# Kernel tuning notes

Hardware: AMD Instinct MI355X
Metric: run time of the kernel (lower is better)

Reference implementation:

```python
import jax, jax.numpy as jnp
import numpy as np

B, NP, K, E = 8, 4096, 1024, 262144   # graphs, nodes/graph, topk keep, edges
N = B * NP
EPS = 1e-5


def _glorot(k, fi, fo):
    lim = float(np.sqrt(6.0 / (fi + fo)))
    return jax.random.uniform(k, (fi, fo), jnp.float32, -lim, lim)


def setup_inputs() -> dict:
    key = jax.random.key(0)
    ks = jax.random.split(key, 16)
    pos = jax.random.normal(ks[0], (N, 3), jnp.float32)
    epg = E // B
    src = jax.random.randint(ks[1], (E,), 0, NP)
    dst = jax.random.randint(ks[2], (E,), 0, NP)
    off = jnp.repeat(jnp.arange(B) * NP, epg)   # edges stay within their graph
    edge_index = jnp.stack([src + off, dst + off]).astype(jnp.int32)
    batch = jnp.repeat(jnp.arange(B, dtype=jnp.int32), NP)
    inp = {"pos": pos, "edge_index": edge_index, "batch": batch,
           "p": jax.random.normal(ks[3], (3,), jnp.float32)}
    dims = [3, 64, 128, 128, 256, 512]
    for i in range(5):
        fi, fo = dims[i], dims[i + 1]
        inp[f"W{i+1}"] = _glorot(ks[4 + i], fi, fo)
        inp[f"b{i+1}"] = jnp.zeros((fo,), jnp.float32)
        inp[f"g{i+1}"] = jnp.ones((fo,), jnp.float32)
        inp[f"be{i+1}"] = jnp.zeros((fo,), jnp.float32)
    for i, (fi, fo) in enumerate([(512, 256), (256, 256), (256, 100)]):
        inp[f"fw{i+1}"] = _glorot(ks[9 + i], fi, fo)
        inp[f"fb{i+1}"] = jnp.zeros((fo,), jnp.float32)
    return inp


def _bn(x, g, b):
    # BatchNorm1d in training mode: batch stats over the node dim
    m = jnp.mean(x, 0)
    v = jnp.var(x, 0)
    return (x - m) * jax.lax.rsqrt(v + EPS) * g + b


def _gcn(x, src, dst, ew, W, bb, n):
    # GCNConv with add_self_loops=True, symmetric normalization.
    h = x @ W                                              # [n, out]
    deg = jax.ops.segment_sum(ew, dst, num_segments=n) + 1.0  # +1 self-loop
    dinv = jax.lax.rsqrt(deg)
    norm = dinv[src] * ew * dinv[dst]                      # masked edges -> 0
    agg = jax.ops.segment_sum(h[src] * norm[:, None], dst, num_segments=n)
    return agg + h * (dinv * dinv)[:, None] + bb           # self-loop term + bias


def _forward(pos, p, W1, b1, g1, be1, W2, b2, g2, be2, W3, b3, g3, be3,
             W4, b4, g4, be4, W5, b5, g5, be5, fw1, fb1, fw2, fb2, fw3, fb3,
             edge_index):
    # --- TopKPooling(ratio=1024): projection score, tanh, top-k per graph ---
    s = jnp.tanh(pos @ p / jnp.linalg.norm(p))             # [N]
    vals, idx = jax.lax.top_k(s.reshape(B, NP), K)         # [B,K]
    perm = (idx + (jnp.arange(B) * NP)[:, None]).reshape(-1)
    x = pos[perm] * vals.reshape(-1)[:, None]              # gate kept nodes
    Nn = B * K
    remap = jnp.full((N,), -1, jnp.int32).at[perm].set(jnp.arange(Nn, dtype=jnp.int32))
    src, dst = remap[edge_index[0]], remap[edge_index[1]]
    valid = (src >= 0) & (dst >= 0)
    ew = valid.astype(x.dtype)                             # 0-weight == removed edge
    src = jnp.where(valid, src, 0)
    dst = jnp.where(valid, dst, 0)
    for (W, bb, g, be) in ((W1, b1, g1, be1), (W2, b2, g2, be2),
                           (W3, b3, g3, be3), (W4, b4, g4, be4),
                           (W5, b5, g5, be5)):
        x = jax.nn.relu(_bn(_gcn(x, src, dst, ew, W, bb, Nn), g, be))
    # --- global sum pooling (torch_scatter default reduce='sum') ---
    batch_new = jnp.repeat(jnp.arange(B), K)
    x = jax.ops.segment_sum(x, batch_new, num_segments=B)  # [B,512]
    x = jax.nn.relu(x @ fw1 + fb1)
    x = jax.nn.relu(x @ fw2 + fb2)
    return jax.nn.log_softmax(x @ fw3 + fb3, axis=-1)      # [B,100]


def reference(pos, edge_index, batch, p, W1, b1, g1, be1, W2, b2, g2, be2,
              W3, b3, g3, be3, W4, b4, g4, be4, W5, b5, g5, be5,
              fw1, fb1, fw2, fb2, fw3, fb3):
    del batch  # graph ids are the fixed contiguous layout encoded in B, NP, K
    return _forward(pos, p, W1, b1, g1, be1, W2, b2, g2, be2, W3, b3, g3, be3,
                    W4, b4, g4, be4, W5, b5, g5, be5,
                    fw1, fb1, fw2, fb2, fw3, fb3, edge_index)
```

## Files before the change

kernel.cpp:

```cpp
#include <hip/hip_runtime.h>
#include <math.h>

#define NTOT 32768
#define NPG  4096
#define BGR  8
#define KK   1024
#define NN   8192
#define NE   262144

typedef __attribute__((ext_vector_type(8))) short bf16x8;
typedef __attribute__((ext_vector_type(4))) float f32x4;

static __device__ __forceinline__ unsigned short f2bf(float f) {
    unsigned u = __float_as_uint(f);
    return (unsigned short)((u + 0x7fffu + ((u >> 16) & 1u)) >> 16);
}
static __device__ __forceinline__ float bf2f(unsigned short b) {
    return __uint_as_float(((unsigned)b) << 16);
}

__global__ __launch_bounds__(1024) void k_topk2(const float* __restrict__ pos,
                                                const float* __restrict__ p,
                                                int* __restrict__ remap,
                                                float* __restrict__ x0f,
                                                unsigned short* __restrict__ Ab0,
                                                int* __restrict__ deg,
                                                int* __restrict__ cursor) {
    __shared__ unsigned skey[NPG];
    __shared__ float sval[NPG];
    __shared__ int hist[256];
    __shared__ int Sarr[256];
    __shared__ int wsum[16];
    __shared__ int s_bin, s_above;

    const int g = blockIdx.x, tid = threadIdx.x;
    const int lane = tid & 63, wid = tid >> 6;
    deg[g * KK + tid] = 0;
    cursor[g * KK + tid] = 0;
    const float p0 = p[0], p1 = p[1], p2 = p[2];
    const float invn = 1.0f / sqrtf(p0 * p0 + p1 * p1 + p2 * p2);

    for (int i = tid; i < NPG; i += 1024) {
        const float* pp = pos + (size_t)(g * NPG + i) * 3;
        float s = tanhf((pp[0] * p0 + pp[1] * p1 + pp[2] * p2) * invn);
        sval[i] = s;
        unsigned b = __float_as_uint(s);
        skey[i] = (b & 0x80000000u) ? ~b : (b | 0x80000000u);
    }
    __syncthreads();

    unsigned prefix = 0;
    int needed = KK;
    for (int r = 0; r < 4; ++r) {
        const int sh = 24 - 8 * r;
        if (tid < 256) hist[tid] = 0;
        __syncthreads();
        for (int i = tid; i < NPG; i += 1024) {
            unsigned k = skey[i];
            bool act = (r == 0) || ((k >> (sh + 8)) == prefix);
            if (act) atomicAdd(&hist[(k >> sh) & 255u], 1);
        }
        __syncthreads();
        if (wid == 0) {
            int h0 = hist[4 * lane + 0], h1 = hist[4 * lane + 1];
            int h2 = hist[4 * lane + 2], h3 = hist[4 * lane + 3];
            int l3 = h3, l2 = h2 + l3, l1 = h1 + l2, l0 = h0 + l1;
            int t = l0;
            for (int off = 1; off < 64; off <<= 1) {
                int n = __shfl_down(t, off, 64);
                if (lane + off < 64) t += n;
            }
            int hi = t - l0;
            Sarr[4 * lane + 0] = l0 + hi;
            Sarr[4 * lane + 1] = l1 + hi;
            Sarr[4 * lane + 2] = l2 + hi;
            Sarr[4 * lane + 3] = l3 + hi;
        }
        __syncthreads();
        if (tid < 256) {
            int Sb = Sarr[tid];
            int Sb1 = (tid < 255) ? Sarr[tid + 1] : 0;
            if (Sb >= needed && Sb1 < needed) { s_bin = tid; s_above = Sb1; }
        }
        __syncthreads();
        needed -= s_above;
        prefix = (prefix << 8) | (unsigned)s_bin;
        __syncthreads();
    }
    const unsigned Tkey = prefix;
    const int needTies = needed;

    int tiebase = 0, keepbase = 0;
    for (int c = 0; c < 4; ++c) {
        const int i = c * 1024 + tid;
        const unsigned k = skey[i];
        const int tie = (k == Tkey) ? 1 : 0;
        int v = tie;
        for (int off = 1; off < 64; off <<= 1) {
            int n = __shfl_up(v, off, 64);
            if (lane >= off) v += n;
        }
        if (lane == 63) wsum[wid] = v;
        __syncthreads();
        if (wid == 0) {
            int w = (lane < 16) ? wsum[lane] : 0;
            for (int off = 1; off < 16; off <<= 1) {
                int n = __shfl_up(w, off, 64);
                if (lane >= off) w += n;
            }
            if (lane < 16) wsum[lane] = w;
        }
        __syncthreads();
        const int trank = tiebase + v + (wid > 0 ? wsum[wid - 1] : 0) - tie;
        const int ttot = wsum[15];
        const int keep = (k > Tkey) || (tie && trank < needTies);
        __syncthreads();
        int u = keep;
        for (int off = 1; off < 64; off <<= 1) {
            int n = __shfl_up(u, off, 64);
            if (lane >= off) u += n;
        }
        if (lane == 63) wsum[wid] = u;
        __syncthreads();
        if (wid == 0) {
            int w = (lane < 16) ? wsum[lane] : 0;
            for (int off = 1; off < 16; off <<= 1) {
                int n = __shfl_up(w, off, 64);
                if (lane >= off) w += n;
            }
            if (lane < 16) wsum[lane] = w;
        }
        __syncthreads();
        const int kincl = u + (wid > 0 ? wsum[wid - 1] : 0);
        const int ktot = wsum[15];
        if (keep) {
            int nn = g * KK + keepbase + kincl - 1;
            remap[g * NPG + i] = nn;
            float val = sval[i];
            const float* pp = pos + (size_t)(g * NPG + i) * 3;
            float v0 = pp[0] * val, v1 = pp[1] * val, v2 = pp[2] * val;
            x0f[(size_t)nn * 3 + 0] = v0;
            x0f[(size_t)nn * 3 + 1] = v1;
            x0f[(size_t)nn * 3 + 2] = v2;
            unsigned short* rw = Ab0 + (size_t)nn * 32;
            ushort4 a = make_ushort4(f2bf(v0), f2bf(v1), f2bf(v2), 0);
            ushort4 z = make_ushort4(0, 0, 0, 0);
            *(ushort4*)(rw) = a;
#pragma unroll
            for (int t = 1; t < 8; ++t) *(ushort4*)(rw + 4 * t) = z;
        } else {
            remap[g * NPG + i] = -1;
        }
        tiebase += ttot;
        keepbase += ktot;
        __syncthreads();
    }
}

__global__ void k_deg(const int* __restrict__ ei, const int* __restrict__ remap,
                      int* __restrict__ deg) {
    int e = blockIdx.x * blockDim.x + threadIdx.x;
    if (e >= NE) return;
    int s = remap[ei[e]];
    int d = remap[ei[NE + e]];
    if (s >= 0 && d >= 0) atomicAdd(&deg[d], 1);
}

__global__ __launch_bounds__(1024) void k_scan(const int* __restrict__ deg,
                                               int* __restrict__ rowptr) {
    __shared__ int part[1024];
    const int tid = threadIdx.x;
    const int base = tid * 8;
    int loc[8];
    int s = 0;
#pragma unroll
    for (int i = 0; i < 8; ++i) { loc[i] = s; s += deg[base + i]; }
    part[tid] = s;
    __syncthreads();
    for (int off = 1; off < 1024; off <<= 1) {
        int v = (tid >= off) ? part[tid - off] : 0;
        __syncthreads();
        part[tid] += v;
        __syncthreads();
    }
    int pre = (tid > 0) ? part[tid - 1] : 0;
#pragma unroll
    for (int i = 0; i < 8; ++i) rowptr[base + i] = pre + loc[i];
    if (tid == 1023) rowptr[NN] = pre + s;
}

__global__ void k_place2(const int* __restrict__ ei, const int* __restrict__ remap,
                         const int* __restrict__ deg, const int* __restrict__ rowptr,
                         int* __restrict__ cursor, int* __restrict__ col,
                         float* __restrict__ ew) {
    int e = blockIdx.x * blockDim.x + threadIdx.x;
    if (e >= NE) return;
    int s = remap[ei[e]];
    int d = remap[ei[NE + e]];
    if (s >= 0 && d >= 0) {
        int pos = rowptr[d] + atomicAdd(&cursor[d], 1);
        col[pos] = s;
        ew[pos] = rsqrtf((float)(deg[s] + 1)) * rsqrtf((float)(deg[d] + 1));
    }
}

__global__ void k_wt_all(const float* __restrict__ w0, const float* __restrict__ w1,
                         const float* __restrict__ w2, const float* __restrict__ w3,
                         const float* __restrict__ w4,
                         unsigned short* __restrict__ t0, unsigned short* __restrict__ t1,
                         unsigned short* __restrict__ t2, unsigned short* __restrict__ t3,
                         unsigned short* __restrict__ t4) {
    int i = blockIdx.x * blockDim.x + threadIdx.x;
    const float* W; unsigned short* T; int Kd, Nc, Kpad, base;
    if (i < 2048)        { W = w0; T = t0; Kd = 3;   Nc = 64;  Kpad = 32;  base = 0; }
    else if (i < 10240)  { W = w1; T = t1; Kd = 64;  Nc = 128; Kpad = 64;  base = 2048; }
    else if (i < 26624)  { W = w2; T = t2; Kd = 128; Nc = 128; Kpad = 128; base = 10240; }
    else if (i < 59392)  { W = w3; T = t3; Kd = 128; Nc = 256; Kpad = 128; base = 26624; }
    else if (i < 190464) { W = w4; T = t4; Kd = 256; Nc = 512; Kpad = 256; base = 59392; }
    else return;
    int j = i - base;
    int n = j / Kpad, k = j - n * Kpad;
    float v = (k < Kd) ? W[(size_t)k * Nc + n] : 0.0f;
    T[j] = f2bf(v);
}

__global__ __launch_bounds__(256) void k_mm2(const unsigned short* __restrict__ Ab,
                                             const float* __restrict__ Yin,
                                             const float* __restrict__ scale,
                                             const float* __restrict__ shift,
                                             const unsigned short* __restrict__ WT,
                                             unsigned short* __restrict__ Hb,
                                             int Kd, int Nc) {
    const int lane = threadIdx.x & 63, wid = threadIdx.x >> 6;
    const int bm = blockIdx.x * 64 + (wid >> 1) * 32;
    const int bn = blockIdx.y * 64 + (wid & 1) * 32;
    const int fr = lane & 15;
    const int ko = (lane >> 4) << 3;
    const int row0 = bm + fr;
    const unsigned short* B0 = WT + (size_t)(bn + fr) * Kd + ko;
    const size_t strA = (size_t)16 * Kd;
    f32x4 acc00 = {0,0,0,0}, acc01 = {0,0,0,0}, acc10 = {0,0,0,0}, acc11 = {0,0,0,0};
    for (int k0 = 0; k0 < Kd; k0 += 32) {
        bf16x8 a0, a1;
        if (Yin) {
            const int cc = ko + k0;
            const float4 sc0 = *(const float4*)&scale[cc];
            const float4 sc1 = *(const float4*)&scale[cc + 4];
            const float4 sh0 = *(const float4*)&shift[cc];
            const float4 sh1 = *(const float4*)&shift[cc + 4];
            const float* y0 = Yin + (size_t)row0 * Kd + cc;
            const float* y1 = y0 + strA;
#pragma unroll
            for (int h = 0; h < 2; ++h) {
                const float* yy = h ? y1 : y0;
                float4 u = *(const float4*)yy;
                float4 v = *(const float4*)(yy + 4);
                bf16x8 a;
                a[0] = (short)f2bf(fmaxf(u.x * sc0.x + sh0.x, 0.0f));
                a[1] = (short)f2bf(fmaxf(u.y * sc0.y + sh0.y, 0.0f));
                a[2] = (short)f2bf(fmaxf(u.z * sc0.z + sh0.z, 0.0f));
                a[3] = (short)f2bf(fmaxf(u.w * sc0.w + sh0.w, 0.0f));
                a[4] = (short)f2bf(fmaxf(v.x * sc1.x + sh1.x, 0.0f));
                a[5] = (short)f2bf(fmaxf(v.y * sc1.y + sh1.y, 0.0f));
                a[6] = (short)f2bf(fmaxf(v.z * sc1.z + sh1.z, 0.0f));
                a[7] = (short)f2bf(fmaxf(v.w * sc1.w + sh1.w, 0.0f));
                if (h) a1 = a; else a0 = a;
            }
        } else {
            const unsigned short* A0 = Ab + (size_t)row0 * Kd + ko + k0;
            a0 = *(const bf16x8*)A0;
            a1 = *(const bf16x8*)(A0 + strA);
        }
        bf16x8 b0 = *(const bf16x8*)(B0 + k0);
        bf16x8 b1 = *(const bf16x8*)(B0 + strA + k0);
        acc00 = __builtin_amdgcn_mfma_f32_16x16x32_bf16(b0, a0, acc00, 0, 0, 0);
        acc01 = __builtin_amdgcn_mfma_f32_16x16x32_bf16(b1, a0, acc01, 0, 0, 0);
        acc10 = __builtin_amdgcn_mfma_f32_16x16x32_bf16(b0, a1, acc10, 0, 0, 0);
        acc11 = __builtin_amdgcn_mfma_f32_16x16x32_bf16(b1, a1, acc11, 0, 0, 0);
    }
    const int r = lane & 15;
    const int c4 = (lane >> 4) << 2;
#pragma unroll
    for (int tm = 0; tm < 2; ++tm) {
        const int row = bm + tm * 16 + r;
        const size_t basep = (size_t)row * Nc;
        const f32x4 aL = tm ? acc10 : acc00;
        const f32x4 aR = tm ? acc11 : acc01;
#pragma unroll
        for (int tn = 0; tn < 2; ++tn) {
            const f32x4 a = tn ? aR : aL;
            const int c = bn + tn * 16 + c4;
            *(ushort4*)&Hb[basep + c] = make_ushort4(f2bf(a[0]), f2bf(a[1]),
                                                     f2bf(a[2]), f2bf(a[3]));
        }
    }
}

__global__ __launch_bounds__(256) void k_mm2w(const float* __restrict__ Yin,
                                              const float* __restrict__ scale,
                                              const float* __restrict__ shift,
                                              const unsigned short* __restrict__ WT,
                                              unsigned short* __restrict__ Hb,
                                              int Kd, int Nc) {
    const int lane = threadIdx.x & 63, wid = threadIdx.x >> 6;
    const int bm = blockIdx.x * 64 + (wid >> 1) * 32;
    const int bn = blockIdx.y * 128 + (wid & 1) * 32;
    const int fr = lane & 15;
    const int ko = (lane >> 4) << 3;
    const int row0 = bm + fr;
    const unsigned short* B0 = WT + (size_t)(bn + fr) * Kd + ko;
    const unsigned short* B2 = WT + (size_t)(bn + 64 + fr) * Kd + ko;
    const size_t strA = (size_t)16 * Kd;
    f32x4 acc00 = {0,0,0,0}, acc01 = {0,0,0,0}, acc10 = {0,0,0,0}, acc11 = {0,0,0,0};
    f32x4 acc20 = {0,0,0,0}, acc21 = {0,0,0,0}, acc30 = {0,0,0,0}, acc31 = {0,0,0,0};
    for (int k0 = 0; k0 < Kd; k0 += 32) {
        bf16x8 a0, a1;
        {
            const int cc = ko + k0;
            const float4 sc0 = *(const float4*)&scale[cc];
            const float4 sc1 = *(const float4*)&scale[cc + 4];
            const float4 sh0 = *(const float4*)&shift[cc];
            const float4 sh1 = *(const float4*)&shift[cc + 4];
            const float* y0 = Yin + (size_t)row0 * Kd + cc;
            const float* y1 = y0 + strA;
#pragma unroll
            for (int h = 0; h < 2; ++h) {
                const float* yy = h ? y1 : y0;
                float4 u = *(const float4*)yy;
                float4 v = *(const float4*)(yy + 4);
                bf16x8 a;
                a[0] = (short)f2bf(fmaxf(u.x * sc0.x + sh0.x, 0.0f));
                a[1] = (short)f2bf(fmaxf(u.y * sc0.y + sh0.y, 0.0f));
                a[2] = (short)f2bf(fmaxf(u.z * sc0.z + sh0.z, 0.0f));
                a[3] = (short)f2bf(fmaxf(u.w * sc0.w + sh0.w, 0.0f));
                a[4] = (short)f2bf(fmaxf(v.x * sc1.x + sh1.x, 0.0f));
                a[5] = (short)f2bf(fmaxf(v.y * sc1.y + sh1.y, 0.0f));
                a[6] = (short)f2bf(fmaxf(v.z * sc1.z + sh1.z, 0.0f));
                a[7] = (short)f2bf(fmaxf(v.w * sc1.w + sh1.w, 0.0f));
                if (h) a1 = a; else a0 = a;
            }
        }
        bf16x8 b0 = *(const bf16x8*)(B0 + k0);
        bf16x8 b1 = *(const bf16x8*)(B0 + strA + k0);
        bf16x8 b2 = *(const bf16x8*)(B2 + k0);
        bf16x8 b3 = *(const bf16x8*)(B2 + strA + k0);
        acc00 = __builtin_amdgcn_mfma_f32_16x16x32_bf16(b0, a0, acc00, 0, 0, 0);
        acc01 = __builtin_amdgcn_mfma_f32_16x16x32_bf16(b1, a0, acc01, 0, 0, 0);
        acc10 = __builtin_amdgcn_mfma_f32_16x16x32_bf16(b0, a1, acc10, 0, 0, 0);
        acc11 = __builtin_amdgcn_mfma_f32_16x16x32_bf16(b1, a1, acc11, 0, 0, 0);
        acc20 = __builtin_amdgcn_mfma_f32_16x16x32_bf16(b2, a0, acc20, 0, 0, 0);
        acc21 = __builtin_amdgcn_mfma_f32_16x16x32_bf16(b3, a0, acc21, 0, 0, 0);
        acc30 = __builtin_amdgcn_mfma_f32_16x16x32_bf16(b2, a1, acc30, 0, 0, 0);
        acc31 = __builtin_amdgcn_mfma_f32_16x16x32_bf16(b3, a1, acc31, 0, 0, 0);
    }
    const int r = lane & 15;
    const int c4 = (lane >> 4) << 2;
#pragma unroll
    for (int ct = 0; ct < 2; ++ct) {
#pragma unroll
        for (int tm = 0; tm < 2; ++tm) {
            const int row = bm + tm * 16 + r;
            const size_t basep = (size_t)row * Nc;
            f32x4 aL, aR;
            if (ct == 0) { aL = tm ? acc10 : acc00; aR = tm ? acc11 : acc01; }
            else         { aL = tm ? acc30 : acc20; aR = tm ? acc31 : acc21; }
#pragma unroll
            for (int tn = 0; tn < 2; ++tn) {
                const f32x4 a = tn ? aR : aL;
                const int c = bn + ct * 64 + tn * 16 + c4;
                *(ushort4*)&Hb[basep + c] = make_ushort4(f2bf(a[0]), f2bf(a[1]),
                                                         f2bf(a[2]), f2bf(a[3]));
            }
        }
    }
}

#define BM 64
#define BNT 64
#define BKT 16
__global__ __launch_bounds__(256) void k_mm(const float* __restrict__ A,
                                            const float* __restrict__ W,
                                            float* __restrict__ H, int Kd, int Nc) {
    __shared__ float As[BM][BKT + 1];
    __shared__ float Bs[BKT][BNT + 1];
    const int bm = blockIdx.x * BM;
    const int bn = blockIdx.y * BNT;
    const int tid = threadIdx.x;
    const int tx = tid & 15, ty = tid >> 4;
    float acc[4][4] = {};
    for (int k0 = 0; k0 < Kd; k0 += BKT) {
        for (int t = 0; t < 4; ++t) {
            int i = tid + t * 256;
            int m = i >> 4, k = i & 15;
            As[m][k] = (k0 + k < Kd) ? A[(size_t)(bm + m) * Kd + k0 + k] : 0.0f;
        }
        for (int t = 0; t < 4; ++t) {
            int i = tid + t * 256;
            int k = i >> 6, n = i & 63;
            Bs[k][n] = (k0 + k < Kd) ? W[(size_t)(k0 + k) * Nc + bn + n] : 0.0f;
        }
        __syncthreads();
        for (int k = 0; k < BKT; ++k) {
            float a[4], b[4];
#pragma unroll
            for (int i = 0; i < 4; ++i) a[i] = As[ty * 4 + i][k];
#pragma unroll
            for (int j = 0; j < 4; ++j) b[j] = Bs[k][tx * 4 + j];
#pragma unroll
            for (int i = 0; i < 4; ++i)
#pragma unroll
                for (int j = 0; j < 4; ++j) acc[i][j] += a[i] * b[j];
        }
        __syncthreads();
    }
#pragma unroll
    for (int i = 0; i < 4; ++i)
        *(float4*)&H[(size_t)(bm + ty * 4 + i) * Nc + bn + tx * 4] =
            make_float4(acc[i][0], acc[i][1], acc[i][2], acc[i][3]);
}

#define BN1_ROWS 16
#define BN1_CHUNKS (NN / BN1_ROWS)
__global__ __launch_bounds__(256) void k_gfuse(const unsigned short* __restrict__ Hb,
                                               const float* __restrict__ Hf,
                                               const int* __restrict__ rowptr,
                                               const int* __restrict__ col,
                                               const float* __restrict__ ew,
                                               const int* __restrict__ deg,
                                               const float* __restrict__ bias,
                                               float* __restrict__ Y,
                                               float* __restrict__ psum,
                                               float* __restrict__ psq, int Nc) {
    __shared__ float4 ls[256], lq[256];
    const int CHB = (Nc < 128) ? Nc : 128;
    const int CB = Nc / CHB;
    const int chunk = blockIdx.x / CB;
    const int cb = blockIdx.x - chunk * CB;
    const int QPB = CHB >> 2;
    const int tid = threadIdx.x;
    const int q = tid & (QPB - 1);
    const int rg = tid / QPB;
    const int NRG = 256 / QPB;
    const int RPT = BN1_ROWS / NRG;
    const int c = cb * CHB + (q << 2);
    const float4 b4 = *(const float4*)&bias[c];
    float4 s4 = make_float4(0, 0, 0, 0), q4 = make_float4(0, 0, 0, 0);
    for (int rr = 0; rr < RPT; ++rr) {
        const int n = chunk * BN1_ROWS + rg * RPT + rr;
        const int j0 = rowptr[n], j1 = rowptr[n + 1];
        const float inv = 1.0f / (float)(deg[n] + 1);
        float4 acc;
        if (Hb) {
            ushort4 hv = *(const ushort4*)&Hb[(size_t)n * Nc + c];
            acc = make_float4(bf2f(hv.x), bf2f(hv.y), bf2f(hv.z), bf2f(hv.w));
        } else {
            acc = *(const float4*)&Hf[(size_t)n * Nc + c];
        }
        acc.x = acc.x * inv + b4.x;
        acc.y = acc.y * inv + b4.y;
        acc.z = acc.z * inv + b4.z;
        acc.w = acc.w * inv + b4.w;
        if (Hb) {
            for (int j = j0; j < j1; ++j) {
                const float w = ew[j];
                ushort4 hv = *(const ushort4*)&Hb[(size_t)col[j] * Nc + c];
                acc.x += bf2f(hv.x) * w; acc.y += bf2f(hv.y) * w;
                acc.z += bf2f(hv.z) * w; acc.w += bf2f(hv.w) * w;
            }
        } else {
            for (int j = j0; j < j1; ++j) {
                const float w = ew[j];
                const float4 hv = *(const float4*)&Hf[(size_t)col[j] * Nc + c];
                acc.x += hv.x * w; acc.y += hv.y * w; acc.z += hv.z * w; acc.w += hv.w * w;
            }
        }
        *(float4*)&Y[(size_t)n * Nc + c] = acc;
        s4.x += acc.x; s4.y += acc.y; s4.z += acc.z; s4.w += acc.w;
        q4.x += acc.x * acc.x; q4.y += acc.y * acc.y;
        q4.z += acc.z * acc.z; q4.w += acc.w * acc.w;
    }
    ls[tid] = s4; lq[tid] = q4;
    __syncthreads();
    for (int st = 128; st >= QPB; st >>= 1) {
        if (tid < st) {
            float4 a = ls[tid], b = ls[tid + st];
            ls[tid] = make_float4(a.x + b.x, a.y + b.y, a.z + b.z, a.w + b.w);
            float4 e = lq[tid], f = lq[tid + st];
            lq[tid] = make_float4(e.x + f.x, e.y + f.y, e.z + f.z, e.w + f.w);
        }
        __syncthreads();
    }
    if (tid < QPB) {
        *(float4*)&psum[(size_t)chunk * Nc + c] = ls[tid];
        *(float4*)&psq[(size_t)chunk * Nc + c] = lq[tid];
    }
}

__global__ __launch_bounds__(256) void k_bn2p(const float* __restrict__ psum,
                                              const float* __restrict__ psq,
                                              const float* __restrict__ g,
                                              const float* __restrict__ be,
                                              float* __restrict__ scale,
                                              float* __restrict__ shift, int Nc) {
    __shared__ float ss[256], sq[256];
    const int c = blockIdx.x;
    const int t = threadIdx.x;
    float s = 0.0f, q = 0.0f;
    for (int b = t; b < BN1_CHUNKS; b += 256) {
        s += psum[(size_t)b * Nc + c];
        q += psq[(size_t)b * Nc + c];
    }
    ss[t] = s; sq[t] = q;
    __syncthreads();
    for (int st = 128; st > 0; st >>= 1) {
        if (t < st) { ss[t] += ss[t + st]; sq[t] += sq[t + st]; }
        __syncthreads();
    }
    if (t == 0) {
        double mean = (double)ss[0] / 8192.0;
        double var = (double)sq[0] / 8192.0 - mean * mean;
        float sc = (float)((double)g[c] / sqrt(var + 1e-5));
        scale[c] = sc;
        shift[c] = be[c] - (float)mean * sc;
    }
}

__global__ void k_bnapply(float* x, const float* __restrict__ scale,
                          const float* __restrict__ shift, int Nc) {
    int i = blockIdx.x * blockDim.x + threadIdx.x;
    int c4 = i & ((Nc >> 2) - 1);
    float4 v = ((const float4*)x)[i];
    float4 sc = ((const float4*)scale)[c4];
    float4 sh = ((const float4*)shift)[c4];
    v.x = fmaxf(v.x * sc.x + sh.x, 0.0f);
    v.y = fmaxf(v.y * sc.y + sh.y, 0.0f);
    v.z = fmaxf(v.z * sc.z + sh.z, 0.0f);
    v.w = fmaxf(v.w * sc.w + sh.w, 0.0f);
    ((float4*)x)[i] = v;
}

#define PR 32
__global__ __launch_bounds__(256) void k_pool_af(const float* __restrict__ Y,
                                                 const float* __restrict__ scale,
                                                 const float* __restrict__ shift,
                                                 float* __restrict__ part) {
    __shared__ float4 red[128];
    const int g = blockIdx.x >> 5;
    const int rs = blockIdx.x & 31;
    const int half = threadIdx.x >> 7;
    const int q = threadIdx.x & 127;
    const float4 sc = *(const float4*)&scale[4 * q];
    const float4 sh = *(const float4*)&shift[4 * q];
    const float* xp = Y + (size_t)(g * KK + rs * PR + half * 16) * 512 + 4 * q;
    float4 s = make_float4(0, 0, 0, 0);
#pragma unroll
    for (int rr = 0; rr < 16; ++rr) {
        float4 v = *(const float4*)(xp + (size_t)rr * 512);
        s.x += fmaxf(v.x * sc.x + sh.x, 0.0f);
        s.y += fmaxf(v.y * sc.y + sh.y, 0.0f);
        s.z += fmaxf(v.z * sc.z + sh.z, 0.0f);
        s.w += fmaxf(v.w * sc.w + sh.w, 0.0f);
    }
    if (half == 1) red[q] = s;
    __syncthreads();
    if (half == 0) {
        float4 t = red[q];
        s.x += t.x; s.y += t.y; s.z += t.z; s.w += t.w;
        *(float4*)&part[(size_t)blockIdx.x * 512 + 4 * q] = s;
    }
}

__global__ __launch_bounds__(256) void k_pool(const float* __restrict__ x, float* pooled) {
    __shared__ float red[4][64];
    int g = blockIdx.x >> 3;
    int c0 = (blockIdx.x & 7) * 64;
    int c = threadIdx.x & 63;
    int rp = threadIdx.x >> 6;
    float s = 0;
    for (int r = rp; r < KK; r += 4)
        s += x[(size_t)(g * KK + r) * 512 + c0 + c];
    red[rp][c] = s;
    __syncthreads();
    if (rp == 0)
        pooled[g * 512 + c0 + c] = red[0][c] + red[1][c] + red[2][c] + red[3][c];
}

__global__ __launch_bounds__(256) void k_fc1s(const float* __restrict__ part,
                                              const float* __restrict__ fw1,
                                              float* __restrict__ part2) {
    __shared__ float pooled_s[32];
    __shared__ float red[256];
    const int g = blockIdx.x, s = blockIdx.y, tid = threadIdx.x;
    const int j = tid & 31;
    const int i = tid >> 5;
    float p = 0;
    for (int a = i; a < 32; a += 8)
        p += part[(size_t)(g * 32 + a) * 512 + 32 * s + j];
    red[tid] = p;
    __syncthreads();
    if (tid < 32) {
        float t = red[tid];
        for (int i2 = 1; i2 < 8; ++i2) t += red[i2 * 32 + tid];
        pooled_s[tid] = t;
    }
    __syncthreads();
    float acc = 0;
    const float* wp = fw1 + (size_t)(32 * s) * 256 + tid;
#pragma unroll
    for (int k = 0; k < 32; ++k) acc += pooled_s[k] * wp[k * 256];
    part2[(size_t)(g * 16 + s) * 256 + tid] = acc;
}

__global__ __launch_bounds__(256) void k_fc2s(const float* __restrict__ part2,
                                              const float* __restrict__ fb1,
                                              const float* __restrict__ fw2,
                                              float* __restrict__ part3) {
    __shared__ float t1s[256];
    const int g = blockIdx.x, s = blockIdx.y, tid = threadIdx.x;
    float a1 = fb1[tid];
    for (int i = 0; i < 16; ++i) a1 += part2[(size_t)(g * 16 + i) * 256 + tid];
    t1s[tid] = fmaxf(a1, 0.0f);
    __syncthreads();
    float acc = 0;
    const float* wp = fw2 + (size_t)(32 * s) * 256 + tid;
#pragma unroll
    for (int k = 0; k < 32; ++k) acc += t1s[32 * s + k] * wp[k * 256];
    part3[(size_t)(g * 8 + s) * 256 + tid] = acc;
}

__global__ __launch_bounds__(256) void k_fc3f(const float* __restrict__ part3,
                                              const float* __restrict__ fb2,
                                              const float* __restrict__ fw3,
                                              const float* __restrict__ fb3,
                                              float* __restrict__ out) {
    __shared__ float t2s[256];
    __shared__ float red[256];
    __shared__ float logits[100];
    const int g = blockIdx.x, tid = threadIdx.x;
    float a2 = fb2[tid];
    for (int i = 0; i < 8; ++i) a2 += part3[(size_t)(g * 8 + i) * 256 + tid];
    t2s[tid] = fmaxf(a2, 0.0f);
    __syncthreads();
    float v = -INFINITY;
    if (tid < 100) {
        float a3 = fb3[tid];
        for (int k = 0; k < 256; ++k) a3 += t2s[k] * fw3[k * 100 + tid];
        logits[tid] = a3;
        v = a3;
    }
    red[tid] = v;
    __syncthreads();
    for (int s = 128; s > 0; s >>= 1) {
        if (tid < s) red[tid] = fmaxf(red[tid], red[tid + s]);
        __syncthreads();
    }
    float mx = red[0];
    __syncthreads();
    red[tid] = (tid < 100) ? expf(logits[tid] - mx) : 0.0f;
    __syncthreads();
    for (int s = 128; s > 0; s >>= 1) {
        if (tid < s) red[tid] += red[tid + s];
        __syncthreads();
    }
    float lse = logf(red[0]);
    if (tid < 100) out[g * 100 + tid] = logits[tid] - mx - lse;
}

__global__ void k_fc(const float* __restrict__ in, const float* __restrict__ W,
                     const float* __restrict__ bias, float* out, int fi, int fo) {
    __shared__ float row[512];
    int g = blockIdx.x, tid = threadIdx.x;
    for (int k = tid; k < fi; k += blockDim.x) row[k] = in[g * fi + k];
    __syncthreads();
    if (tid < fo) {
        float acc = bias[tid];
        for (int k = 0; k < fi; ++k) acc += row[k] * W[k * fo + tid];
        out[g * fo + tid] = acc > 0.0f ? acc : 0.0f;
    }
}

__global__ __launch_bounds__(256) void k_fc23(const float* __restrict__ t1,
                                              const float* __restrict__ fw2,
                                              const float* __restrict__ fb2,
                                              const float* __restrict__ fw3,
                                              const float* __restrict__ fb3,
                                              float* __restrict__ out) {
    __shared__ float row[256];
    __shared__ float t2s[256];
    __shared__ float red[256];
    __shared__ float logits[100];
    const int g = blockIdx.x, tid = threadIdx.x;
    row[tid] = t1[g * 256 + tid];
    __syncthreads();
    float acc = fb2[tid];
    for (int k = 0; k < 256; ++k) acc += row[k] * fw2[k * 256 + tid];
    t2s[tid] = acc > 0.0f ? acc : 0.0f;
    __syncthreads();
    float v = -INFINITY;
    if (tid < 100) {
        float a3 = fb3[tid];
        for (int k = 0; k < 256; ++k) a3 += t2s[k] * fw3[k * 100 + tid];
        logits[tid] = a3;
        v = a3;
    }
    red[tid] = v;
    __syncthreads();
    for (int s = 128; s > 0; s >>= 1) {
        if (tid < s) red[tid] = fmaxf(red[tid], red[tid + s]);
        __syncthreads();
    }
    float mx = red[0];
    __syncthreads();
    red[tid] = (tid < 100) ? expf(logits[tid] - mx) : 0.0f;
    __syncthreads();
    for (int s = 128; s > 0; s >>= 1) {
        if (tid < s) red[tid] += red[tid + s];
        __syncthreads();
    }
    float lse = logf(red[0]);
    if (tid < 100) out[g * 100 + tid] = logits[tid] - mx - lse;
}

extern "C" void kernel_launch(void* const* d_in, const int* in_sizes, int n_in,
                              void* d_out, int out_size, void* d_ws, size_t ws_size,
                              hipStream_t stream) {
    const float* pos = (const float*)d_in[0];
    const int* ei = (const int*)d_in[1];
    const float* p = (const float*)d_in[3];
    const float *W[5], *bb[5], *gg[5], *be[5];
    for (int i = 0; i < 5; ++i) {
        W[i]  = (const float*)d_in[4 + 4 * i];
        bb[i] = (const float*)d_in[5 + 4 * i];
        gg[i] = (const float*)d_in[6 + 4 * i];
        be[i] = (const float*)d_in[7 + 4 * i];
    }
    const float* fw1 = (const float*)d_in[24]; const float* fb1 = (const float*)d_in[25];
    const float* fw2 = (const float*)d_in[26]; const float* fb2 = (const float*)d_in[27];
    const float* fw3 = (const float*)d_in[28]; const float* fb3 = (const float*)d_in[29];
    float* out = (float*)d_out;

    const int fins[5]  = {3, 64, 128, 128, 256};
    const int kpads[5] = {32, 64, 128, 128, 256};
    const int fouts[5] = {64, 128, 128, 256, 512};

    size_t off = 0;
    char* base = (char*)d_ws;
    auto alloc = [&](size_t bytes) { char* q = base + off; off += (bytes + 255) & ~(size_t)255; return q; };

    float* Y      = (float*)alloc((size_t)NN * 512 * 4);
    float* Hf     = (float*)alloc((size_t)NN * 512 * 4);
    int*   remap  = (int*)alloc((size_t)NTOT * 4);
    int*   deg    = (int*)alloc(NN * 4);
    int*   cursor = (int*)alloc(NN * 4);
    int*   rowptr = (int*)alloc((NN + 1) * 4);
    int*   ecol   = (int*)alloc((size_t)NE * 4);
    float* ew     = (float*)alloc((size_t)NE * 4);
    float* psum   = (float*)alloc((size_t)BN1_CHUNKS * 512 * 4);
    float* psq    = (float*)alloc((size_t)BN1_CHUNKS * 512 * 4);
    float* scale  = (float*)alloc(512 * 4);
    float* shift  = (float*)alloc(512 * 4);
    float* pooled = (float*)alloc(8 * 512 * 4);
    float* t1     = (float*)alloc(8 * 256 * 4);
    unsigned short* Ab0 = (unsigned short*)alloc((size_t)NN * 32 * 2);
    float* part   = (float*)alloc((size_t)256 * 512 * 4);
    float* part2  = (float*)alloc((size_t)8 * 16 * 256 * 4);
    float* part3  = (float*)alloc((size_t)8 * 8 * 256 * 4);
    unsigned short* WT[5];
    for (int l = 0; l < 5; ++l) WT[l] = (unsigned short*)alloc((size_t)fouts[l] * kpads[l] * 2);
    unsigned short* Hb = (unsigned short*)Hf;
    const bool mfma = (ws_size >= off);

    k_topk2<<<BGR, 1024, 0, stream>>>(pos, p, remap, Y, Ab0, deg, cursor);
    k_deg<<<NE / 256, 256, 0, stream>>>(ei, remap, deg);
    k_scan<<<1, 1024, 0, stream>>>(deg, rowptr);
    k_place2<<<NE / 256, 256, 0, stream>>>(ei, remap, deg, rowptr, cursor, ecol, ew);

    if (mfma) {
        k_wt_all<<<(190464 + 255) / 256, 256, 0, stream>>>(W[0], W[1], W[2], W[3], W[4],
                                                           WT[0], WT[1], WT[2], WT[3], WT[4]);
        for (int l = 0; l < 5; ++l) {
            int fo = fouts[l];
            if (l == 0) {
                dim3 mg(NN / 64, fo / 64);
                k_mm2<<<mg, 256, 0, stream>>>(Ab0, nullptr, nullptr, nullptr,
                                              WT[l], Hb, kpads[l], fo);
            } else if (fo == 512) {
                dim3 mg(NN / 64, fo / 128);
                k_mm2w<<<mg, 256, 0, stream>>>(Y, scale, shift, WT[l], Hb, kpads[l], fo);
            } else {
                dim3 mg(NN / 64, fo / 64);
                k_mm2<<<mg, 256, 0, stream>>>(nullptr, Y, scale, shift,
                                              WT[l], Hb, kpads[l], fo);
            }
            int cbs = (fo < 128) ? 1 : fo / 128;
            k_gfuse<<<BN1_CHUNKS * cbs, 256, 0, stream>>>(Hb, nullptr, rowptr, ecol, ew,
                                                          deg, bb[l], Y, psum, psq, fo);
            k_bn2p<<<fo, 256, 0, stream>>>(psum, psq, gg[l], be[l], scale, shift, fo);
        }
        k_pool_af<<<256, 256, 0, stream>>>(Y, scale, shift, part);
        k_fc1s<<<dim3(8, 16), 256, 0, stream>>>(part, fw1, part2);
        k_fc2s<<<dim3(8, 8), 256, 0, stream>>>(part2, fb1, fw2, part3);
        k_fc3f<<<8, 256, 0, stream>>>(part3, fb2, fw3, fb3, out);
    } else {
        for (int l = 0; l < 5; ++l) {
            int fi = fins[l], fo = fouts[l];
            dim3 mg(NN / BM, fo / BNT);
            k_mm<<<mg, 256, 0, stream>>>(Y, W[l], Hf, fi, fo);
            int cbs = (fo < 128) ? 1 : fo / 128;
            k_gfuse<<<BN1_CHUNKS * cbs, 256, 0, stream>>>(nullptr, Hf, rowptr, ecol, ew,
                                                          deg, bb[l], Y, psum, psq, fo);
            k_bn2p<<<fo, 256, 0, stream>>>(psum, psq, gg[l], be[l], scale, shift, fo);
            k_bnapply<<<(NN * fo) / 1024, 256, 0, stream>>>(Y, scale, shift, fo);
        }
        k_pool<<<64, 256, 0, stream>>>(Y, pooled);
        k_fc<<<8, 256, 0, stream>>>(pooled, fw1, fb1, t1, 512, 256);
        k_fc23<<<8, 256, 0, stream>>>(t1, fw2, fb2, fw3, fb3, out);
    }
}
```

Measured before the change: 176.0 us.

## Fuse degree, scan and CSR placement into per-graph top-k kernel using LDS

```diff
diff --git a/kernel.cpp b/kernel.cpp
--- a/kernel.cpp
+++ b/kernel.cpp
@@ -7,6 +7,7 @@
 #define KK   1024
 #define NN   8192
 #define NE   262144
+#define EPG  (NE / BGR)
 
 typedef __attribute__((ext_vector_type(8))) short bf16x8;
 typedef __attribute__((ext_vector_type(4))) float f32x4;
@@ -19,24 +20,29 @@
     return __uint_as_float(((unsigned)b) << 16);
 }
 
-__global__ __launch_bounds__(1024) void k_topk2(const float* __restrict__ pos,
+__global__ __launch_bounds__(1024) void k_topk3(const float* __restrict__ pos,
                                                 const float* __restrict__ p,
-                                                int* __restrict__ remap,
+                                                const int* __restrict__ ei,
                                                 float* __restrict__ x0f,
                                                 unsigned short* __restrict__ Ab0,
                                                 int* __restrict__ deg,
-                                                int* __restrict__ cursor) {
+                                                int* __restrict__ rowptr,
+                                                int* __restrict__ ecol,
+                                                float* __restrict__ ew) {
     __shared__ unsigned skey[NPG];
     __shared__ float sval[NPG];
+    __shared__ int remap_l[NPG];
     __shared__ int hist[256];
     __shared__ int Sarr[256];
     __shared__ int wsum[16];
     __shared__ int s_bin, s_above;
+    __shared__ int deg_l[KK];
+    __shared__ int rowp_l[KK];
+    __shared__ int cur_l[KK];
+    __shared__ int scanb[1024];
 
     const int g = blockIdx.x, tid = threadIdx.x;
     const int lane = tid & 63, wid = tid >> 6;
-    deg[g * KK + tid] = 0;
-    cursor[g * KK + tid] = 0;
     const float p0 = p[0], p1 = p[1], p2 = p[2];
     const float invn = 1.0f / sqrtf(p0 * p0 + p1 * p1 + p2 * p2);
 
@@ -135,7 +141,7 @@
         const int ktot = wsum[15];
         if (keep) {
             int nn = g * KK + keepbase + kincl - 1;
-            remap[g * NPG + i] = nn;
+            remap_l[i] = nn;
             float val = sval[i];
             const float* pp = pos + (size_t)(g * NPG + i) * 3;
             float v0 = pp[0] * val, v1 = pp[1] * val, v2 = pp[2] * val;
@@ -149,58 +155,50 @@
 #pragma unroll
             for (int t = 1; t < 8; ++t) *(ushort4*)(rw + 4 * t) = z;
         } else {
-            remap[g * NPG + i] = -1;
+            remap_l[i] = -1;
         }
         tiebase += ttot;
         keepbase += ktot;
         __syncthreads();
     }
-}
-
-__global__ void k_deg(const int* __restrict__ ei, const int* __restrict__ remap,
-                      int* __restrict__ deg) {
-    int e = blockIdx.x * blockDim.x + threadIdx.x;
-    if (e >= NE) return;
-    int s = remap[ei[e]];
-    int d = remap[ei[NE + e]];
-    if (s >= 0 && d >= 0) atomicAdd(&deg[d], 1);
-}
-
-__global__ __launch_bounds__(1024) void k_scan(const int* __restrict__ deg,
-                                               int* __restrict__ rowptr) {
-    __shared__ int part[1024];
-    const int tid = threadIdx.x;
-    const int base = tid * 8;
-    int loc[8];
-    int s = 0;
-#pragma unroll
-    for (int i = 0; i < 8; ++i) { loc[i] = s; s += deg[base + i]; }
-    part[tid] = s;
-    __syncthreads();
-    for (int off = 1; off < 1024; off <<= 1) {
-        int v = (tid >= off) ? part[tid - off] : 0;
-        __syncthreads();
-        part[tid] += v;
-        __syncthreads();
-    }
-    int pre = (tid > 0) ? part[tid - 1] : 0;
-#pragma unroll
-    for (int i = 0; i < 8; ++i) rowptr[base + i] = pre + loc[i];
-    if (tid == 1023) rowptr[NN] = pre + s;
-}
-
-__global__ void k_place2(const int* __restrict__ ei, const int* __restrict__ remap,
-                         const int* __restrict__ deg, const int* __restrict__ rowptr,
-                         int* __restrict__ cursor, int* __restrict__ col,
-                         float* __restrict__ ew) {
-    int e = blockIdx.x * blockDim.x + threadIdx.x;
-    if (e >= NE) return;
-    int s = remap[ei[e]];
-    int d = remap[ei[NE + e]];
-    if (s >= 0 && d >= 0) {
-        int pos = rowptr[d] + atomicAdd(&cursor[d], 1);
-        col[pos] = s;
-        ew[pos] = rsqrtf((float)(deg[s] + 1)) * rsqrtf((float)(deg[d] + 1));
+
+    deg_l[tid] = 0;
+    __syncthreads();
+    const int ebase = g * EPG;
+    for (int it = 0; it < EPG; it += 1024) {
+        int e = ebase + it + tid;
+        int snn = remap_l[ei[e] - g * NPG];
+        int dnn = remap_l[ei[NE + e] - g * NPG];
+        if (snn >= 0 && dnn >= 0) atomicAdd(&deg_l[dnn - g * KK], 1);
+    }
+    __syncthreads();
+    deg[g * KK + tid] = deg_l[tid];
+
+    int myv = deg_l[tid];
+    scanb[tid] = myv;
+    __syncthreads();
+    for (int off2 = 1; off2 < 1024; off2 <<= 1) {
+        int vv = (tid >= off2) ? scanb[tid - off2] : 0;
+        __syncthreads();
+        scanb[tid] += vv;
+        __syncthreads();
+    }
+    rowp_l[tid] = scanb[tid] - myv;
+    cur_l[tid] = 0;
+    rowptr[g * KK + tid] = ebase + rowp_l[tid];
+    __syncthreads();
+
+    for (int it = 0; it < EPG; it += 1024) {
+        int e = ebase + it + tid;
+        int snn = remap_l[ei[e] - g * NPG];
+        int dnn = remap_l[ei[NE + e] - g * NPG];
+        if (snn >= 0 && dnn >= 0) {
+            int dloc = dnn - g * KK;
+            int pos = ebase + rowp_l[dloc] + atomicAdd(&cur_l[dloc], 1);
+            ecol[pos] = snn;
+            ew[pos] = rsqrtf((float)(deg_l[snn - g * KK] + 1)) *
+                      rsqrtf((float)(deg_l[dloc] + 1));
+        }
     }
 }
 
@@ -447,8 +445,9 @@
     float4 s4 = make_float4(0, 0, 0, 0), q4 = make_float4(0, 0, 0, 0);
     for (int rr = 0; rr < RPT; ++rr) {
         const int n = chunk * BN1_ROWS + rg * RPT + rr;
-        const int j0 = rowptr[n], j1 = rowptr[n + 1];
-        const float inv = 1.0f / (float)(deg[n] + 1);
+        const int dn = deg[n];
+        const int j0 = rowptr[n], j1 = j0 + dn;
+        const float inv = 1.0f / (float)(dn + 1);
         float4 acc;
         if (Hb) {
             ushort4 hv = *(const ushort4*)&Hb[(size_t)n * Nc + c];
@@ -749,10 +748,8 @@
 
     float* Y      = (float*)alloc((size_t)NN * 512 * 4);
     float* Hf     = (float*)alloc((size_t)NN * 512 * 4);
-    int*   remap  = (int*)alloc((size_t)NTOT * 4);
     int*   deg    = (int*)alloc(NN * 4);
-    int*   cursor = (int*)alloc(NN * 4);
-    int*   rowptr = (int*)alloc((NN + 1) * 4);
+    int*   rowptr = (int*)alloc(NN * 4);
     int*   ecol   = (int*)alloc((size_t)NE * 4);
     float* ew     = (float*)alloc((size_t)NE * 4);
     float* psum   = (float*)alloc((size_t)BN1_CHUNKS * 512 * 4);
@@ -770,10 +767,7 @@
     unsigned short* Hb = (unsigned short*)Hf;
     const bool mfma = (ws_size >= off);
 
-    k_topk2<<<BGR, 1024, 0, stream>>>(pos, p, remap, Y, Ab0, deg, cursor);
-    k_deg<<<NE / 256, 256, 0, stream>>>(ei, remap, deg);
-    k_scan<<<1, 1024, 0, stream>>>(deg, rowptr);
-    k_place2<<<NE / 256, 256, 0, stream>>>(ei, remap, deg, rowptr, cursor, ecol, ew);
+    k_topk3<<<BGR, 1024, 0, stream>>>(pos, p, ei, Y, Ab0, deg, rowptr, ecol, ew);
 
     if (mfma) {
         k_wt_all<<<(190464 + 255) / 256, 256, 0, stream>>>(W[0], W[1], W[2], W[3], W[4],
```

Measured after the change: 188.8 us. +7.3%, slower.
